# Performance work log

Measured on AMD Instinct MI355X. Metric: run time of the kernel, lower is better.

Reference implementation:

```python
import jax, jax.numpy as jnp
import numpy as np

T, S, B, D, H = 1024, 1024, 4, 512, 8
HD = D // H
DFF = 2048
W = 16  # sliding-window half-width -> band of 2W+1 keys per query
EPS = 1e-5
SCALE = 1.0 / float(np.sqrt(HD))


def setup_inputs():
    key = jax.random.key(0)
    ks = jax.random.split(key, 16)
    sc = 0.02
    def nrm(k, sh):
        return jax.random.normal(k, sh, jnp.float32) * sc
    z = lambda sh: jnp.zeros(sh, jnp.float32)
    o = lambda sh: jnp.ones(sh, jnp.float32)
    return {
        "tgt": nrm(ks[0], (T, B, D)),
        "memory": nrm(ks[1], (S, B, D)),
        "in_proj_w": nrm(ks[2], (3 * D, D)), "in_proj_b": z((3 * D,)),
        "out_proj_w": nrm(ks[3], (D, D)), "out_proj_b": z((D,)),
        "sw_q_w": nrm(ks[4], (D, D)), "sw_q_b": z((D,)),
        "sw_k_w": nrm(ks[5], (D, D)), "sw_k_b": z((D,)),
        "sw_v_w": nrm(ks[6], (D, D)), "sw_v_b": z((D,)),
        "sw_o_w": nrm(ks[7], (D, D)), "sw_o_b": z((D,)),
        "lin1_w": nrm(ks[8], (DFF, D)), "lin1_b": z((DFF,)),
        "lin2_w": nrm(ks[9], (D, DFF)), "lin2_b": z((D,)),
        "n1_g": o((D,)), "n1_b": z((D,)),
        "n2_g": o((D,)), "n2_b": z((D,)),
        "n3_g": o((D,)), "n3_b": z((D,)),
    }


def _ln(x, g, b):
    m = jnp.mean(x, -1, keepdims=True)
    v = jnp.mean(jnp.square(x - m), -1, keepdims=True)
    return (x - m) * jax.lax.rsqrt(v + EPS) * g + b


def _heads(x):  # [L,B,D] -> [L,B,H,HD]
    return x.reshape(x.shape[0], B, H, HD)


def _self_attn(x, wqkv, bqkv, wo, bo):
    # nn.MultiheadAttention, seq-first layout [T,B,D]
    qkv = jnp.einsum('tbd,ed->tbe', x, wqkv) + bqkv
    q, k, v = (_heads(a) for a in jnp.split(qkv, 3, axis=-1))
    scores = jnp.einsum('tbhd,sbhd->bhts', q, k) * SCALE
    attn = jax.nn.softmax(scores, -1)
    out = jnp.einsum('bhts,sbhd->tbhd', attn, v).reshape(T, B, D)
    return jnp.einsum('tbd,ed->tbe', out, wo) + bo


def _sliding_window_attn(x, mem, wq, bq, wk, bk, wv, bv, wo, bo):
    # banded cross-attention: query i attends to memory keys |i-j| <= W
    q = _heads(jnp.einsum('tbd,ed->tbe', x, wq) + bq)    # [T,B,H,HD]
    k = _heads(jnp.einsum('sbd,ed->sbe', mem, wk) + bk)  # [S,B,H,HD]
    v = _heads(jnp.einsum('sbd,ed->sbe', mem, wv) + bv)
    idx = jnp.arange(T)[:, None] + jnp.arange(-W, W + 1)[None, :]  # [T,2W+1]
    valid = (idx >= 0) & (idx < S)
    idxc = jnp.clip(idx, 0, S - 1)
    kb = k[idxc]  # [T,2W+1,B,H,HD] banded key gather (no dense TxS mask)
    vb = v[idxc]
    scores = jnp.einsum('tbhd,twbhd->bhtw', q, kb) * SCALE
    scores = jnp.where(valid[None, None, :, :], scores, -jnp.inf)
    attn = jax.nn.softmax(scores, -1)
    out = jnp.einsum('bhtw,twbhd->tbhd', attn, vb).reshape(T, B, D)
    return jnp.einsum('tbd,ed->tbe', out, wo) + bo


def reference(tgt, memory, in_proj_w, in_proj_b, out_proj_w, out_proj_b,
              sw_q_w, sw_q_b, sw_k_w, sw_k_b, sw_v_w, sw_v_b, sw_o_w, sw_o_b,
              lin1_w, lin1_b, lin2_w, lin2_b,
              n1_g, n1_b, n2_g, n2_b, n3_g, n3_b):
    # norm_first=False (post-norm) path, pattern='sliding_window', eval mode (dropout=0)
    x = tgt
    x = _ln(x + _self_attn(x, in_proj_w, in_proj_b, out_proj_w, out_proj_b), n1_g, n1_b)
    x = _ln(x + _sliding_window_attn(x, memory, sw_q_w, sw_q_b, sw_k_w, sw_k_b,
                                     sw_v_w, sw_v_b, sw_o_w, sw_o_b), n2_g, n2_b)
    h = jax.nn.relu(jnp.einsum('tbd,fd->tbf', x, lin1_w) + lin1_b)
    ff = jnp.einsum('tbf,df->tbd', h, lin2_w) + lin2_b
    x = _ln(x + ff, n3_g, n3_b)
    return x
```

## Files before the change

kernel.cpp:

```cpp
#include <hip/hip_runtime.h>

typedef unsigned short u16;
typedef unsigned int u32;

#define BATCH 4
#define NTOK 4096
#define SCALE_ATTN 0.125f

typedef float f32x4 __attribute__((ext_vector_type(4)));
typedef __bf16 bf16x8 __attribute__((ext_vector_type(8)));

__device__ __forceinline__ float b2f(u16 s) { return __uint_as_float(((u32)s) << 16); }
__device__ __forceinline__ u16 f2bf(float f) {
    u32 u = __float_as_uint(f);
    u += 0x7FFFu + ((u >> 16) & 1u);
    return (u16)(u >> 16);
}
__device__ __forceinline__ u32 pk2(float x, float y) {
    return (u32)f2bf(x) | ((u32)f2bf(y) << 16);
}
__device__ __forceinline__ u32 pk2t(float x, float y) {
    return (__float_as_uint(x) >> 16) | (__float_as_uint(y) & 0xFFFF0000u);
}
__device__ __forceinline__ uint4 pack8(float4 a, float4 b) {
    uint4 r;
    r.x = pk2(a.x, a.y); r.y = pk2(a.z, a.w);
    r.z = pk2(b.x, b.y); r.w = pk2(b.z, b.w);
    return r;
}
__device__ __forceinline__ f32x4 mfma16(uint4 a, uint4 b, f32x4 c) {
    return __builtin_amdgcn_mfma_f32_16x16x32_bf16(
        __builtin_bit_cast(bf16x8, a), __builtin_bit_cast(bf16x8, b), c, 0, 0, 0);
}

struct CvtTable {
    const float* src[10];
    u32 start[10];
};
__global__ __launch_bounds__(256) void cvt_bf16_kernel(CvtTable tab, u16* __restrict__ dst)
{
    u32 i8 = (blockIdx.x * 256u + threadIdx.x) * 8u;
    int t = 0;
    #pragma unroll
    for (int k = 1; k < 10; ++k) t += (i8 >= tab.start[k]) ? 1 : 0;
    const float* s = tab.src[t] + (i8 - tab.start[t]);
    float4 f0 = *(const float4*)s;
    float4 f1 = *(const float4*)(s + 4);
    *(uint4*)(dst + i8) = pack8(f0, f1);
}

template<int BM, int BN>
__global__ __launch_bounds__(256) void gemm_lds_kernel(
    const u16* __restrict__ A, const u16* __restrict__ B,
    const float* __restrict__ bias, u16* __restrict__ C,
    int M, int N, int K, int relu)
{
    constexpr int WMF = BM / 32;
    constexpr int WNF = BN / 32;
    constexpr int AIW = BM / 32;
    constexpr int BIW = BN / 32;

    __shared__ u16 As[BM * 64];
    __shared__ u16 Bs[BN * 64];

    const int tid = threadIdx.x;
    const int wave = tid >> 6, lane = tid & 63;
    const int lm = lane & 15, quad = lane >> 4;
    const int m0 = blockIdx.y * BM, n0 = blockIdx.x * BN;
    const int wr = wave >> 1, wc = wave & 1;
    const int lk = (lane >> 4) * 8;

    f32x4 acc[WMF][WNF] = {};

    for (int k0 = 0; k0 < K; k0 += 64) {
        #pragma unroll
        for (int t = 0; t < AIW; ++t) {
            int j = wave * AIW + t;
            int i = j >> 1, c = j & 1;
            const u16* gp = A + (size_t)(m0 + i * 16 + lm) * K + k0 + c * 32 + lk;
            __builtin_amdgcn_global_load_lds(
                (const __attribute__((address_space(1))) u32*)gp,
                (__attribute__((address_space(3))) u32*)(As + j * 512), 16, 0, 0);
        }
        #pragma unroll
        for (int t = 0; t < BIW; ++t) {
            int j = wave * BIW + t;
            int i = j >> 1, c = j & 1;
            const u16* gp = B + (size_t)(n0 + i * 16 + lm) * K + k0 + c * 32 + lk;
            __builtin_amdgcn_global_load_lds(
                (const __attribute__((address_space(1))) u32*)gp,
                (__attribute__((address_space(3))) u32*)(Bs + j * 512), 16, 0, 0);
        }
        __syncthreads();

        #pragma unroll
        for (int kk = 0; kk < 2; ++kk) {
            uint4 af[WMF], bf[WNF];
            #pragma unroll
            for (int i2 = 0; i2 < WMF; ++i2) {
                int g = wr * WMF + i2;
                af[i2] = *(const uint4*)(As + ((g * 8 + kk * 4 + quad) * 16 + lm) * 8);
            }
            #pragma unroll
            for (int j2 = 0; j2 < WNF; ++j2) {
                int g = wc * WNF + j2;
                bf[j2] = *(const uint4*)(Bs + ((g * 8 + kk * 4 + quad) * 16 + lm) * 8);
            }
            #pragma unroll
            for (int i2 = 0; i2 < WMF; ++i2)
                #pragma unroll
                for (int j2 = 0; j2 < WNF; ++j2)
                    acc[i2][j2] = mfma16(af[i2], bf[j2], acc[i2][j2]);
        }
        __syncthreads();
    }

    #pragma unroll
    for (int j2 = 0; j2 < WNF; ++j2) {
        int cg = n0 + (wc * WNF + j2) * 16 + lm;
        float bv = bias ? bias[cg] : 0.f;
        #pragma unroll
        for (int i2 = 0; i2 < WMF; ++i2) {
            #pragma unroll
            for (int r = 0; r < 4; ++r) {
                int rg = m0 + (wr * WMF + i2) * 16 + quad * 4 + r;
                float v = acc[i2][j2][r] + bv;
                if (relu) v = fmaxf(v, 0.f);
                C[(size_t)rg * N + cg] = f2bf(v);
            }
        }
    }
}

__global__ __launch_bounds__(256) void add_ln_kernel(
    const u16* __restrict__ a, const void* __restrict__ r,
    const float* __restrict__ g, const float* __restrict__ be,
    void* __restrict__ out, int r_f32, int out_f32)
{
    const int row = blockIdx.x, tid = threadIdx.x;
    u32 av = *(const u32*)(a + (size_t)row * 512 + tid * 2);
    float r0, r1;
    if (r_f32) {
        float2 rv = *(const float2*)((const float*)r + (size_t)row * 512 + tid * 2);
        r0 = rv.x; r1 = rv.y;
    } else {
        u32 rv = *(const u32*)((const u16*)r + (size_t)row * 512 + tid * 2);
        r0 = b2f((u16)(rv & 0xFFFFu)); r1 = b2f((u16)(rv >> 16));
    }
    float v0 = b2f((u16)(av & 0xFFFFu)) + r0;
    float v1 = b2f((u16)(av >> 16)) + r1;
    float s = v0 + v1, q = v0 * v0 + v1 * v1;
    #pragma unroll
    for (int m = 1; m < 64; m <<= 1) { s += __shfl_xor(s, m); q += __shfl_xor(q, m); }
    __shared__ float ss[4], qq[4];
    int wave = tid >> 6, lane = tid & 63;
    if (lane == 0) { ss[wave] = s; qq[wave] = q; }
    __syncthreads();
    s = ss[0] + ss[1] + ss[2] + ss[3];
    q = qq[0] + qq[1] + qq[2] + qq[3];
    float mean = s * (1.f / 512.f);
    float var = q * (1.f / 512.f) - mean * mean;
    float rstd = rsqrtf(var + 1e-5f);
    float2 gv = *(const float2*)(g + tid * 2);
    float2 bv = *(const float2*)(be + tid * 2);
    float o0 = (v0 - mean) * rstd * gv.x + bv.x;
    float o1 = (v1 - mean) * rstd * gv.y + bv.y;
    if (out_f32) {
        float2 ov; ov.x = o0; ov.y = o1;
        *(float2*)((float*)out + (size_t)row * 512 + tid * 2) = ov;
    } else {
        *(u32*)((u16*)out + (size_t)row * 512 + tid * 2) = pk2(o0, o1);
    }
}

__global__ __launch_bounds__(256) void self_attn_kernel(
    const u16* __restrict__ qkv, u16* __restrict__ o)
{
    const int qb = blockIdx.x;
    const int bh = blockIdx.y;
    const int b = bh >> 3, h = bh & 7;
    const int tid = threadIdx.x;
    const int lane = tid & 63, wave = tid >> 6;
    const int lm = lane & 15, quad = lane >> 4;

    __shared__ u16 Ks[64 * 64];
    __shared__ u16 Vt[64][72];

    const int qrow0 = qb * 64 + wave * 16;
    const u16* qp = qkv + ((size_t)(qrow0 + lm) * BATCH + b) * 1536 + h * 64;
    uint4 qf0 = *(const uint4*)(qp + quad * 8);
    uint4 qf1 = *(const uint4*)(qp + 32 + quad * 8);

    f32x4 o4[4] = {};
    float m_s = -1e30f, l_s = 0.f;

    for (int c0 = 0; c0 < 1024; c0 += 64) {
        #pragma unroll
        for (int t2 = 0; t2 < 2; ++t2) {
            int j = wave * 2 + t2;
            int g = j >> 1, c = j & 1;
            const u16* gp = qkv + ((size_t)(c0 + g * 16 + lm) * BATCH + b) * 1536
                            + 512 + h * 64 + c * 32 + quad * 8;
            __builtin_amdgcn_global_load_lds(
                (const __attribute__((address_space(1))) u32*)gp,
                (__attribute__((address_space(3))) u32*)(Ks + j * 512), 16, 0, 0);
        }
        #pragma unroll
        for (int i = 0; i < 2; ++i) {
            int c = tid + i * 256;
            int key = c & 63, dv = (c >> 6) * 8;
            uint4 u = *(const uint4*)(
                qkv + ((size_t)(c0 + key) * BATCH + b) * 1536 + 1024 + h * 64 + dv);
            Vt[dv + 0][key] = (u16)(u.x & 0xFFFFu);
            Vt[dv + 1][key] = (u16)(u.x >> 16);
            Vt[dv + 2][key] = (u16)(u.y & 0xFFFFu);
            Vt[dv + 3][key] = (u16)(u.y >> 16);
            Vt[dv + 4][key] = (u16)(u.z & 0xFFFFu);
            Vt[dv + 5][key] = (u16)(u.z >> 16);
            Vt[dv + 6][key] = (u16)(u.w & 0xFFFFu);
            Vt[dv + 7][key] = (u16)(u.w >> 16);
        }
        __syncthreads();

        f32x4 s[4] = {};
        #pragma unroll
        for (int t = 0; t < 4; ++t) {
            uint4 k0 = *(const uint4*)(Ks + t * 1024 + quad * 128 + lm * 8);
            uint4 k1 = *(const uint4*)(Ks + t * 1024 + 512 + quad * 128 + lm * 8);
            s[t] = mfma16(k0, qf0, s[t]);
            s[t] = mfma16(k1, qf1, s[t]);
        }

        float mx = -1e30f;
        #pragma unroll
        for (int t = 0; t < 4; ++t)
            #pragma unroll
            for (int r = 0; r < 4; ++r) {
                s[t][r] *= SCALE_ATTN;
                mx = fmaxf(mx, s[t][r]);
            }
        mx = fmaxf(mx, __shfl_xor(mx, 16));
        mx = fmaxf(mx, __shfl_xor(mx, 32));
        float mn = fmaxf(m_s, mx);
        float alpha = __expf(m_s - mn);
        m_s = mn;
        float ps = 0.f;
        u32 pkx[4], pky[4];
        #pragma unroll
        for (int t = 0; t < 4; ++t) {
            float p0 = __expf(s[t][0] - mn);
            float p1 = __expf(s[t][1] - mn);
            float p2 = __expf(s[t][2] - mn);
            float p3 = __expf(s[t][3] - mn);
            ps += (p0 + p1) + (p2 + p3);
            pkx[t] = pk2t(p0, p1);
            pky[t] = pk2t(p2, p3);
        }
        ps += __shfl_xor(ps, 16);
        ps += __shfl_xor(ps, 32);
        l_s = l_s * alpha + ps;
        float av[4];
        #pragma unroll
        for (int r = 0; r < 4; ++r) av[r] = __shfl(alpha, quad * 20 + r);
        #pragma unroll
        for (int t = 0; t < 4; ++t)
            #pragma unroll
            for (int r = 0; r < 4; ++r) o4[t][r] *= av[r];

        #pragma unroll
        for (int kh = 0; kh < 2; ++kh) {
            int src1 = lm + 32 * (quad & 1);
            int src2 = src1 + 16;
            u32 xA = (u32)__shfl((int)pkx[2 * kh], src1);
            u32 xB = (u32)__shfl((int)pkx[2 * kh + 1], src1);
            u32 yA = (u32)__shfl((int)pky[2 * kh], src1);
            u32 yB = (u32)__shfl((int)pky[2 * kh + 1], src1);
            u32 zA = (u32)__shfl((int)pkx[2 * kh], src2);
            u32 zB = (u32)__shfl((int)pkx[2 * kh + 1], src2);
            u32 wA = (u32)__shfl((int)pky[2 * kh], src2);
            u32 wB = (u32)__shfl((int)pky[2 * kh + 1], src2);
            bool hiq = quad >= 2;
            uint4 pf;
            pf.x = hiq ? xB : xA;
            pf.y = hiq ? yB : yA;
            pf.z = hiq ? zB : zA;
            pf.w = hiq ? wB : wA;
            #pragma unroll
            for (int t = 0; t < 4; ++t) {
                uint4 vf = *(const uint4*)(&Vt[t * 16 + lm][kh * 32 + quad * 8]);
                o4[t] = mfma16(pf, vf, o4[t]);
            }
        }
        __syncthreads();
    }

    float linv = 1.f / l_s;
    float lv[4];
    #pragma unroll
    for (int r = 0; r < 4; ++r) lv[r] = __shfl(linv, quad * 20 + r);
    #pragma unroll
    for (int t = 0; t < 4; ++t) {
        #pragma unroll
        for (int r = 0; r < 4; ++r) {
            int row = qrow0 + quad * 4 + r;
            o[((size_t)row * BATCH + b) * 512 + h * 64 + t * 16 + lm] =
                f2bf(o4[t][r] * lv[r]);
        }
    }
}

__global__ __launch_bounds__(256) void sw_attn_kernel(
    const u16* __restrict__ q2, const u16* __restrict__ k2,
    const u16* __restrict__ v2, u16* __restrict__ o)
{
    const int idx = blockIdx.x * 256 + threadIdx.x;
    const int h = idx & 7;
    const int tb = idx >> 3;
    const int b = tb & 3;
    const int t = tb >> 2;
    const u16* qp = q2 + (size_t)tb * 512 + h * 64;

    float q[64];
    #pragma unroll
    for (int d8 = 0; d8 < 8; ++d8) {
        uint4 u = *(const uint4*)(qp + d8 * 8);
        q[d8 * 8 + 0] = b2f((u16)(u.x & 0xFFFFu)); q[d8 * 8 + 1] = b2f((u16)(u.x >> 16));
        q[d8 * 8 + 2] = b2f((u16)(u.y & 0xFFFFu)); q[d8 * 8 + 3] = b2f((u16)(u.y >> 16));
        q[d8 * 8 + 4] = b2f((u16)(u.z & 0xFFFFu)); q[d8 * 8 + 5] = b2f((u16)(u.z >> 16));
        q[d8 * 8 + 6] = b2f((u16)(u.w & 0xFFFFu)); q[d8 * 8 + 7] = b2f((u16)(u.w >> 16));
    }
    __shared__ float sbuf[256][33];
    float* s = sbuf[threadIdx.x];

    float mx = -3.0e38f;
    for (int w = 0; w < 33; ++w) {
        int j = t - 16 + w;
        bool valid = (j >= 0) && (j < 1024);
        int jc = valid ? j : 0;
        const u16* kp = k2 + ((size_t)jc * BATCH + b) * 512 + h * 64;
        float acc = 0.f;
        #pragma unroll
        for (int d8 = 0; d8 < 8; ++d8) {
            uint4 u = *(const uint4*)(kp + d8 * 8);
            acc += q[d8 * 8 + 0] * b2f((u16)(u.x & 0xFFFFu));
            acc += q[d8 * 8 + 1] * b2f((u16)(u.x >> 16));
            acc += q[d8 * 8 + 2] * b2f((u16)(u.y & 0xFFFFu));
            acc += q[d8 * 8 + 3] * b2f((u16)(u.y >> 16));
            acc += q[d8 * 8 + 4] * b2f((u16)(u.z & 0xFFFFu));
            acc += q[d8 * 8 + 5] * b2f((u16)(u.z >> 16));
            acc += q[d8 * 8 + 6] * b2f((u16)(u.w & 0xFFFFu));
            acc += q[d8 * 8 + 7] * b2f((u16)(u.w >> 16));
        }
        float svw = valid ? acc * SCALE_ATTN : -3.0e38f;
        s[w] = svw;
        mx = fmaxf(mx, svw);
    }
    float l = 0.f;
    for (int w = 0; w < 33; ++w) {
        float p = __expf(s[w] - mx);
        s[w] = p;
        l += p;
    }
    float inv = 1.f / l;

    float ov[64];
    #pragma unroll
    for (int d = 0; d < 64; ++d) ov[d] = 0.f;
    for (int w = 0; w < 33; ++w) {
        int j = t - 16 + w;
        int jc = j < 0 ? 0 : (j > 1023 ? 1023 : j);
        float p = s[w];
        const u16* vp = v2 + ((size_t)jc * BATCH + b) * 512 + h * 64;
        #pragma unroll
        for (int d8 = 0; d8 < 8; ++d8) {
            uint4 u = *(const uint4*)(vp + d8 * 8);
            ov[d8 * 8 + 0] += p * b2f((u16)(u.x & 0xFFFFu));
            ov[d8 * 8 + 1] += p * b2f((u16)(u.x >> 16));
            ov[d8 * 8 + 2] += p * b2f((u16)(u.y & 0xFFFFu));
            ov[d8 * 8 + 3] += p * b2f((u16)(u.y >> 16));
            ov[d8 * 8 + 4] += p * b2f((u16)(u.z & 0xFFFFu));
            ov[d8 * 8 + 5] += p * b2f((u16)(u.z >> 16));
            ov[d8 * 8 + 6] += p * b2f((u16)(u.w & 0xFFFFu));
            ov[d8 * 8 + 7] += p * b2f((u16)(u.w >> 16));
        }
    }
    u16* op = o + (size_t)tb * 512 + h * 64;
    #pragma unroll
    for (int d2 = 0; d2 < 32; ++d2) {
        *(u32*)(op + d2 * 2) = pk2(ov[2 * d2] * inv, ov[2 * d2 + 1] * inv);
    }
}

static inline void gemm128(hipStream_t st, const u16* A, const u16* B, const float* bias,
                           u16* C, int M, int N, int K, int relu)
{
    dim3 g(N / 128, M / 128);
    gemm_lds_kernel<128, 128><<<g, dim3(256), 0, st>>>(A, B, bias, C, M, N, K, relu);
}
static inline void gemm64(hipStream_t st, const u16* A, const u16* B, const float* bias,
                          u16* C, int M, int N, int K, int relu)
{
    dim3 g(N / 64, M / 64);
    gemm_lds_kernel<64, 64><<<g, dim3(256), 0, st>>>(A, B, bias, C, M, N, K, relu);
}

extern "C" void kernel_launch(void* const* d_in, const int* in_sizes, int n_in,
                              void* d_out, int out_size, void* d_ws, size_t ws_size,
                              hipStream_t stream)
{
    const float* tgt        = (const float*)d_in[0];
    const float* memory     = (const float*)d_in[1];
    const float* in_proj_w  = (const float*)d_in[2];
    const float* in_proj_b  = (const float*)d_in[3];
    const float* out_proj_w = (const float*)d_in[4];
    const float* out_proj_b = (const float*)d_in[5];
    const float* sw_q_w = (const float*)d_in[6];
    const float* sw_q_b = (const float*)d_in[7];
    const float* sw_k_w = (const float*)d_in[8];
    const float* sw_k_b = (const float*)d_in[9];
    const float* sw_v_w = (const float*)d_in[10];
    const float* sw_v_b = (const float*)d_in[11];
    const float* sw_o_w = (const float*)d_in[12];
    const float* sw_o_b = (const float*)d_in[13];
    const float* lin1_w = (const float*)d_in[14];
    const float* lin1_b = (const float*)d_in[15];
    const float* lin2_w = (const float*)d_in[16];
    const float* lin2_b = (const float*)d_in[17];
    const float* n1_g = (const float*)d_in[18];
    const float* n1_b = (const float*)d_in[19];
    const float* n2_g = (const float*)d_in[20];
    const float* n2_b = (const float*)d_in[21];
    const float* n3_g = (const float*)d_in[22];
    const float* n3_b = (const float*)d_in[23];

    u16* ws = (u16*)d_ws;
    u16* qkv  = ws;
    u16* x1   = ws + 6291456;
    u16* bufA = ws + 8388608;
    u16* bufB = ws + 10485760;
    u16* x2   = ws + 12582912;
    u16* q2 = qkv;
    u16* k2 = qkv + 2097152;
    u16* v2 = qkv + 4194304;
    u16* hbuf = qkv;

    u16* wc = ws + 14680064;
    u16* tgtb  = wc;
    u16* memb  = wc + 2097152;
    u16* inpb  = wc + 4194304;
    u16* outpb = wc + 4980736;
    u16* swqb  = wc + 5242880;
    u16* swkb  = wc + 5505024;
    u16* swvb  = wc + 5767168;
    u16* swob  = wc + 6029312;
    u16* l1b   = wc + 6291456;
    u16* l2b   = wc + 7340032;

    CvtTable tab;
    const float* srcs[10] = {tgt, memory, in_proj_w, out_proj_w, sw_q_w,
                             sw_k_w, sw_v_w, sw_o_w, lin1_w, lin2_w};
    const u32 starts[10] = {0, 2097152, 4194304, 4980736, 5242880,
                            5505024, 5767168, 6029312, 6291456, 7340032};
    for (int i = 0; i < 10; ++i) { tab.src[i] = srcs[i]; tab.start[i] = starts[i]; }
    cvt_bf16_kernel<<<dim3(4096), dim3(256), 0, stream>>>(tab, wc);

    gemm128(stream, tgtb, inpb, in_proj_b, qkv, NTOK, 1536, 512, 0);
    self_attn_kernel<<<dim3(16, 32), dim3(256), 0, stream>>>(qkv, bufA);
    gemm64(stream, bufA, outpb, out_proj_b, bufB, NTOK, 512, 512, 0);
    add_ln_kernel<<<dim3(NTOK), dim3(256), 0, stream>>>(bufB, tgt, n1_g, n1_b, x1, 1, 0);
    gemm64(stream, x1, swqb, sw_q_b, q2, NTOK, 512, 512, 0);
    gemm64(stream, memb, swkb, sw_k_b, k2, NTOK, 512, 512, 0);
    gemm64(stream, memb, swvb, sw_v_b, v2, NTOK, 512, 512, 0);
    sw_attn_kernel<<<dim3(128), dim3(256), 0, stream>>>(q2, k2, v2, bufA);
    gemm64(stream, bufA, swob, sw_o_b, bufB, NTOK, 512, 512, 0);
    add_ln_kernel<<<dim3(NTOK), dim3(256), 0, stream>>>(bufB, x1, n2_g, n2_b, x2, 0, 0);
    gemm128(stream, x2, l1b, lin1_b, hbuf, NTOK, 2048, 512, 1);
    gemm64(stream, hbuf, l2b, lin2_b, bufA, NTOK, 512, 2048, 0);
    add_ln_kernel<<<dim3(NTOK), dim3(256), 0, stream>>>(bufA, x2, n3_g, n3_b, d_out, 0, 1);
}
```

Measured before the change: 361.4 us.

## Rewrite sliding-window attention as tiled MFMA kernel with LDS-staged K/V

The sliding-window attention kernel moves from one thread per (token, batch, head) doing scalar dot products to a block per 64-query tile and (batch, head). Each block stages the 112-key band of K into LDS via global_load_lds and a transposed copy of V, then computes scores and P·V with bf16 MFMA instructions. It masks the band, does the softmax with wave shuffles, and writes normalized outputs. This removes redundant global K/V reads per query and the serial scalar FMA chains, at the cost of computing some masked-out scores inside the tile and rounding the probabilities to bf16.

Measured after the change: 308.5 us. 14.6% less time.

```diff
diff --git a/kernel.cpp b/kernel.cpp
--- a/kernel.cpp
+++ b/kernel.cpp
@@ -313,81 +313,135 @@
     const u16* __restrict__ q2, const u16* __restrict__ k2,
     const u16* __restrict__ v2, u16* __restrict__ o)
 {
-    const int idx = blockIdx.x * 256 + threadIdx.x;
-    const int h = idx & 7;
-    const int tb = idx >> 3;
-    const int b = tb & 3;
-    const int t = tb >> 2;
-    const u16* qp = q2 + (size_t)tb * 512 + h * 64;
-
-    float q[64];
-    #pragma unroll
-    for (int d8 = 0; d8 < 8; ++d8) {
-        uint4 u = *(const uint4*)(qp + d8 * 8);
-        q[d8 * 8 + 0] = b2f((u16)(u.x & 0xFFFFu)); q[d8 * 8 + 1] = b2f((u16)(u.x >> 16));
-        q[d8 * 8 + 2] = b2f((u16)(u.y & 0xFFFFu)); q[d8 * 8 + 3] = b2f((u16)(u.y >> 16));
-        q[d8 * 8 + 4] = b2f((u16)(u.z & 0xFFFFu)); q[d8 * 8 + 5] = b2f((u16)(u.z >> 16));
-        q[d8 * 8 + 6] = b2f((u16)(u.w & 0xFFFFu)); q[d8 * 8 + 7] = b2f((u16)(u.w >> 16));
-    }
-    __shared__ float sbuf[256][33];
-    float* s = sbuf[threadIdx.x];
-
-    float mx = -3.0e38f;
-    for (int w = 0; w < 33; ++w) {
-        int j = t - 16 + w;
-        bool valid = (j >= 0) && (j < 1024);
-        int jc = valid ? j : 0;
-        const u16* kp = k2 + ((size_t)jc * BATCH + b) * 512 + h * 64;
-        float acc = 0.f;
-        #pragma unroll
-        for (int d8 = 0; d8 < 8; ++d8) {
-            uint4 u = *(const uint4*)(kp + d8 * 8);
-            acc += q[d8 * 8 + 0] * b2f((u16)(u.x & 0xFFFFu));
-            acc += q[d8 * 8 + 1] * b2f((u16)(u.x >> 16));
-            acc += q[d8 * 8 + 2] * b2f((u16)(u.y & 0xFFFFu));
-            acc += q[d8 * 8 + 3] * b2f((u16)(u.y >> 16));
-            acc += q[d8 * 8 + 4] * b2f((u16)(u.z & 0xFFFFu));
-            acc += q[d8 * 8 + 5] * b2f((u16)(u.z >> 16));
-            acc += q[d8 * 8 + 6] * b2f((u16)(u.w & 0xFFFFu));
-            acc += q[d8 * 8 + 7] * b2f((u16)(u.w >> 16));
-        }
-        float svw = valid ? acc * SCALE_ATTN : -3.0e38f;
-        s[w] = svw;
-        mx = fmaxf(mx, svw);
-    }
-    float l = 0.f;
-    for (int w = 0; w < 33; ++w) {
-        float p = __expf(s[w] - mx);
-        s[w] = p;
-        l += p;
-    }
-    float inv = 1.f / l;
-
-    float ov[64];
-    #pragma unroll
-    for (int d = 0; d < 64; ++d) ov[d] = 0.f;
-    for (int w = 0; w < 33; ++w) {
-        int j = t - 16 + w;
-        int jc = j < 0 ? 0 : (j > 1023 ? 1023 : j);
-        float p = s[w];
-        const u16* vp = v2 + ((size_t)jc * BATCH + b) * 512 + h * 64;
-        #pragma unroll
-        for (int d8 = 0; d8 < 8; ++d8) {
-            uint4 u = *(const uint4*)(vp + d8 * 8);
-            ov[d8 * 8 + 0] += p * b2f((u16)(u.x & 0xFFFFu));
-            ov[d8 * 8 + 1] += p * b2f((u16)(u.x >> 16));
-            ov[d8 * 8 + 2] += p * b2f((u16)(u.y & 0xFFFFu));
-            ov[d8 * 8 + 3] += p * b2f((u16)(u.y >> 16));
-            ov[d8 * 8 + 4] += p * b2f((u16)(u.z & 0xFFFFu));
-            ov[d8 * 8 + 5] += p * b2f((u16)(u.z >> 16));
-            ov[d8 * 8 + 6] += p * b2f((u16)(u.w & 0xFFFFu));
-            ov[d8 * 8 + 7] += p * b2f((u16)(u.w >> 16));
-        }
-    }
-    u16* op = o + (size_t)tb * 512 + h * 64;
-    #pragma unroll
-    for (int d2 = 0; d2 < 32; ++d2) {
-        *(u32*)(op + d2 * 2) = pk2(ov[2 * d2] * inv, ov[2 * d2 + 1] * inv);
+    const int qb = blockIdx.x;
+    const int bh = blockIdx.y;
+    const int b = bh >> 3, h = bh & 7;
+    const int tid = threadIdx.x;
+    const int lane = tid & 63, wave = tid >> 6;
+    const int lm = lane & 15, quad = lane >> 4;
+
+    __shared__ u16 Ks[14 * 512];
+    __shared__ u16 Vt[64][120];
+
+    const int kbase = qb * 64 - 16;
+    const int qrow0 = qb * 64 + wave * 16;
+
+    const u16* qp = q2 + ((size_t)(qrow0 + lm) * BATCH + b) * 512 + h * 64;
+    uint4 qf0 = *(const uint4*)(qp + quad * 8);
+    uint4 qf1 = *(const uint4*)(qp + 32 + quad * 8);
+
+    #pragma unroll
+    for (int t2 = 0; t2 < 4; ++t2) {
+        int j = wave * 4 + t2;
+        if (j < 14) {
+            int g = j >> 1, c = j & 1;
+            int key = kbase + g * 16 + lm;
+            key = min(max(key, 0), 1023);
+            const u16* gp = k2 + ((size_t)key * BATCH + b) * 512 + h * 64
+                            + c * 32 + quad * 8;
+            __builtin_amdgcn_global_load_lds(
+                (const __attribute__((address_space(1))) u32*)gp,
+                (__attribute__((address_space(3))) u32*)(Ks + j * 512), 16, 0, 0);
+        }
+    }
+    #pragma unroll
+    for (int i = 0; i < 4; ++i) {
+        int c = tid + i * 256;
+        if (c < 896) {
+            int key = c >> 3, dv = (c & 7) * 8;
+            int j = kbase + key;
+            j = min(max(j, 0), 1023);
+            uint4 u = *(const uint4*)(v2 + ((size_t)j * BATCH + b) * 512 + h * 64 + dv);
+            Vt[dv + 0][key] = (u16)(u.x & 0xFFFFu);
+            Vt[dv + 1][key] = (u16)(u.x >> 16);
+            Vt[dv + 2][key] = (u16)(u.y & 0xFFFFu);
+            Vt[dv + 3][key] = (u16)(u.y >> 16);
+            Vt[dv + 4][key] = (u16)(u.z & 0xFFFFu);
+            Vt[dv + 5][key] = (u16)(u.z >> 16);
+            Vt[dv + 6][key] = (u16)(u.w & 0xFFFFu);
+            Vt[dv + 7][key] = (u16)(u.w >> 16);
+        }
+    }
+    __syncthreads();
+
+    f32x4 s[4] = {};
+    #pragma unroll
+    for (int t = 0; t < 4; ++t) {
+        int tw = wave + t;
+        uint4 k0 = *(const uint4*)(Ks + (tw * 2 + 0) * 512 + quad * 128 + lm * 8);
+        uint4 k1 = *(const uint4*)(Ks + (tw * 2 + 1) * 512 + quad * 128 + lm * 8);
+        s[t] = mfma16(k0, qf0, s[t]);
+        s[t] = mfma16(k1, qf1, s[t]);
+    }
+
+    float mx = -1e30f;
+    #pragma unroll
+    for (int t = 0; t < 4; ++t) {
+        #pragma unroll
+        for (int r = 0; r < 4; ++r) {
+            int kl = t * 16 + quad * 4 + r;
+            int jj = qrow0 - 16 + kl;
+            int d = kl - lm;
+            bool valid = (d >= 0) && (d <= 32) && (jj >= 0) && (jj < 1024);
+            s[t][r] = valid ? s[t][r] * SCALE_ATTN : -1e30f;
+            mx = fmaxf(mx, s[t][r]);
+        }
+    }
+    mx = fmaxf(mx, __shfl_xor(mx, 16));
+    mx = fmaxf(mx, __shfl_xor(mx, 32));
+    float ps = 0.f;
+    u32 pkx[4], pky[4];
+    #pragma unroll
+    for (int t = 0; t < 4; ++t) {
+        float p0 = __expf(s[t][0] - mx);
+        float p1 = __expf(s[t][1] - mx);
+        float p2 = __expf(s[t][2] - mx);
+        float p3 = __expf(s[t][3] - mx);
+        ps += (p0 + p1) + (p2 + p3);
+        pkx[t] = pk2t(p0, p1);
+        pky[t] = pk2t(p2, p3);
+    }
+    ps += __shfl_xor(ps, 16);
+    ps += __shfl_xor(ps, 32);
+
+    f32x4 o4[4] = {};
+    #pragma unroll
+    for (int kh = 0; kh < 2; ++kh) {
+        int src1 = lm + 32 * (quad & 1);
+        int src2 = src1 + 16;
+        u32 xA = (u32)__shfl((int)pkx[2 * kh], src1);
+        u32 xB = (u32)__shfl((int)pkx[2 * kh + 1], src1);
+        u32 yA = (u32)__shfl((int)pky[2 * kh], src1);
+        u32 yB = (u32)__shfl((int)pky[2 * kh + 1], src1);
+        u32 zA = (u32)__shfl((int)pkx[2 * kh], src2);
+        u32 zB = (u32)__shfl((int)pkx[2 * kh + 1], src2);
+        u32 wA = (u32)__shfl((int)pky[2 * kh], src2);
+        u32 wB = (u32)__shfl((int)pky[2 * kh + 1], src2);
+        bool hiq = quad >= 2;
+        uint4 pf;
+        pf.x = hiq ? xB : xA;
+        pf.y = hiq ? yB : yA;
+        pf.z = hiq ? zB : zA;
+        pf.w = hiq ? wB : wA;
+        #pragma unroll
+        for (int t = 0; t < 4; ++t) {
+            uint4 vf = *(const uint4*)(&Vt[t * 16 + lm][wave * 16 + kh * 32 + quad * 8]);
+            o4[t] = mfma16(pf, vf, o4[t]);
+        }
+    }
+
+    float linv = 1.f / ps;
+    float lv[4];
+    #pragma unroll
+    for (int r = 0; r < 4; ++r) lv[r] = __shfl(linv, quad * 20 + r);
+    #pragma unroll
+    for (int t = 0; t < 4; ++t) {
+        #pragma unroll
+        for (int r = 0; r < 4; ++r) {
+            int row = qrow0 + quad * 4 + r;
+            o[((size_t)row * BATCH + b) * 512 + h * 64 + t * 16 + lm] =
+                f2bf(o4[t][r] * lv[r]);
+        }
     }
 }
 
@@ -471,7 +525,7 @@
     gemm64(stream, x1, swqb, sw_q_b, q2, NTOK, 512, 512, 0);
     gemm64(stream, memb, swkb, sw_k_b, k2, NTOK, 512, 512, 0);
     gemm64(stream, memb, swvb, sw_v_b, v2, NTOK, 512, 512, 0);
-    sw_attn_kernel<<<dim3(128), dim3(256), 0, stream>>>(q2, k2, v2, bufA);
+    sw_attn_kernel<<<dim3(16, 32), dim3(256), 0, stream>>>(q2, k2, v2, bufA);
     gemm64(stream, bufA, swob, sw_o_b, bufB, NTOK, 512, 512, 0);
     add_ln_kernel<<<dim3(NTOK), dim3(256), 0, stream>>>(bufB, x1, n2_g, n2_b, x2, 0, 0);
     gemm128(stream, x2, l1b, lin1_b, hbuf, NTOK, 2048, 512, 1);
```
